# Optimization experiments

Measured on AMD Instinct MI355X. Metric: run time of the kernel, lower is better.

Reference implementation:

```python
import jax, jax.numpy as jnp
import numpy as np

L, H, NH, PF = 2, 256, 8, 512
D = H // NH
SCALE = float(np.sqrt(D))  # transformerCPI scales by sqrt(hid_dim // n_heads)


def layernorm(x, g, b, eps=1e-5):
    m = x.mean(-1, keepdims=True)
    v = ((x - m) ** 2).mean(-1, keepdims=True)
    return (x - m) / jnp.sqrt(v + eps) * g + b


def mha(q, k, v, wq, bq, wk, bk, wv, bv, wo, bo):
    B, Tq, _ = q.shape
    Tk = k.shape[1]
    Q = (q @ wq + bq).reshape(B, Tq, NH, D).transpose(0, 2, 1, 3)  # [B,h,Tq,d]
    K = (k @ wk + bk).reshape(B, Tk, NH, D).transpose(0, 2, 1, 3)
    V = (v @ wv + bv).reshape(B, Tk, NH, D).transpose(0, 2, 1, 3)
    att = jax.nn.softmax(jnp.einsum('bhqd,bhkd->bhqk', Q, K) / SCALE, axis=-1)
    x = jnp.einsum('bhqk,bhkd->bhqd', att, V).transpose(0, 2, 1, 3).reshape(B, Tq, H)
    return x @ wo + bo, att


def setup_inputs() -> dict:
    key = jax.random.key(0)
    ks = iter(jax.random.split(key, 64))
    B, T, S, A = 16, 512, 1024, 64
    p = lambda shape: jax.random.normal(next(ks), shape, jnp.float32) * 0.02
    inp = {
        'trg': jax.random.normal(next(ks), (B, T, A), jnp.float32),
        'src': jax.random.normal(next(ks), (B, S, H), jnp.float32),
        'ft_w': p((A, H)), 'ft_b': jnp.zeros((H,), jnp.float32),
        'fc1_w': p((H, 256)), 'fc1_b': jnp.zeros((256,), jnp.float32),
        'fc2_w': p((256, 2)), 'fc2_b': jnp.zeros((2,), jnp.float32),
        'ln_g': jnp.ones((L, H), jnp.float32), 'ln_b': jnp.zeros((L, H), jnp.float32),
        'pf_w1': p((L, H, PF)), 'pf_b1': jnp.zeros((L, PF), jnp.float32),
        'pf_w2': p((L, PF, H)), 'pf_b2': jnp.zeros((L, H), jnp.float32),
    }
    for pre in ('sa', 'ea'):
        for nm in ('q', 'k', 'v', 'o'):
            inp[f'{pre}_w{nm}'] = p((L, H, H))
            inp[f'{pre}_b{nm}'] = jnp.zeros((L, H), jnp.float32)
    return inp


def reference(trg, src, ft_w, ft_b, sa_wq, sa_bq, sa_wk, sa_bk, sa_wv, sa_bv, sa_wo, sa_bo,
              ea_wq, ea_bq, ea_wk, ea_bk, ea_wv, ea_bv, ea_wo, ea_bo,
              pf_w1, pf_b1, pf_w2, pf_b2, ln_g, ln_b, fc1_w, fc1_b, fc2_w, fc2_b):
    x = trg @ ft_w + ft_b  # [B,T,H]
    att = None
    for l in range(L):  # small fixed layer count
        sa_out, _ = mha(x, x, x, sa_wq[l], sa_bq[l], sa_wk[l], sa_bk[l],
                        sa_wv[l], sa_bv[l], sa_wo[l], sa_bo[l])
        x = layernorm(x + sa_out, ln_g[l], ln_b[l])
        ea_out, att = mha(x, src, src, ea_wq[l], ea_bq[l], ea_wk[l], ea_bk[l],
                          ea_wv[l], ea_bv[l], ea_wo[l], ea_bo[l])
        x = layernorm(x + ea_out, ln_g[l], ln_b[l])
        ff = jax.nn.relu(x @ pf_w1[l] + pf_b1[l]) @ pf_w2[l] + pf_b2[l]
        x = layernorm(x + ff, ln_g[l], ln_b[l])
    # norm-based softmax pooling (vectorized form of the original double loop)
    w = jax.nn.softmax(jnp.linalg.norm(x, axis=2), axis=1)  # [B,T]
    pooled = jnp.einsum('bt,bth->bh', w, x)                 # [B,H]
    label = jax.nn.relu(pooled @ fc1_w + fc1_b) @ fc2_w + fc2_b  # [B,2]
    return label, pooled, att
```

## Files before the change

kernel.cpp:

```cpp
#include <hip/hip_runtime.h>


typedef __bf16 bfrag __attribute__((ext_vector_type(8)));
typedef float f32x4 __attribute__((ext_vector_type(4)));
typedef unsigned int uint4v __attribute__((ext_vector_type(4)));

__device__ __forceinline__ unsigned short f2bf(float x) {
  unsigned u = __float_as_uint(x);
  u += 0x7fff + ((u >> 16) & 1);
  return (unsigned short)(u >> 16);
}
__device__ __forceinline__ float bf2f(unsigned short h) {
  return __uint_as_float((unsigned)h << 16);
}
__device__ __forceinline__ void split2(float x, unsigned short& hi, unsigned short& lo) {
  hi = f2bf(x);
  lo = f2bf(x - bf2f(hi));
}

__global__ __launch_bounds__(256) void wsplit(
    const float* __restrict__ W, short* __restrict__ Th, short* __restrict__ Tl,
    int K, int N)
{
  __shared__ float t[32][33];
  const int n0 = blockIdx.x * 32, k0 = blockIdx.y * 32;
  const int tx = threadIdx.x & 31, ty = threadIdx.x >> 5;
#pragma unroll
  for (int p = 0; p < 4; p++)
    t[ty + p * 8][tx] = W[(size_t)(k0 + ty + p * 8) * N + n0 + tx];
  __syncthreads();
#pragma unroll
  for (int p = 0; p < 4; p++) {
    float v = t[tx][ty + p * 8];
    unsigned short hi, lo; split2(v, hi, lo);
    size_t o = (size_t)(n0 + ty + p * 8) * K + k0 + tx;
    Th[o] = (short)hi; Tl[o] = (short)lo;
  }
}

__global__ __launch_bounds__(256) void xsplit(
    const float* __restrict__ X, short* __restrict__ Xh, short* __restrict__ Xl,
    int n4)
{
  int i = blockIdx.x * 256 + threadIdx.x;
  if (i < n4) {
    float4 v = ((const float4*)X)[i];
    ushort4 h, l;
    split2(v.x, h.x, l.x); split2(v.y, h.y, l.y);
    split2(v.z, h.z, l.z); split2(v.w, h.w, l.w);
    ((ushort4*)Xh)[i] = h; ((ushort4*)Xl)[i] = l;
  }
}

#define GEMM_CORE(Ah_g, Al_g, Bh_g, Bl_g, K)                                   \
  for (int k0 = 0; k0 < K; k0 += 32) {                                         \
    {                                                                          \
      const size_t ga = (size_t)(m0 + srow) * K + k0 + sc4 * 8;                \
      const size_t gb = (size_t)(n0 + srow) * K + k0 + sc4 * 8;                \
      uint4 va_h = *(const uint4*)(Ah_g + ga);                                 \
      uint4 va_l = *(const uint4*)(Al_g + ga);                                 \
      uint4 vb_h = *(const uint4*)(Bh_g + gb);                                 \
      uint4 vb_l = *(const uint4*)(Bl_g + gb);                                 \
      const int so = srow * 40 + sc4 * 8;                                      \
      *(uint4*)(Ah + so) = va_h;  *(uint4*)(Al + so) = va_l;                   \
      *(uint4*)(Bh + so) = vb_h;  *(uint4*)(Bl + so) = vb_l;                   \
    }                                                                          \
    __syncthreads();                                                           \
    bfrag af_h[2], af_l[2], bf_h[2], bf_l[2];                                  \
    _Pragma("unroll")                                                          \
    for (int mi = 0; mi < 2; mi++) {                                           \
      int r = wm * 32 + mi * 16 + l15;                                         \
      af_h[mi] = *(const bfrag*)(Ah + r * 40 + l4 * 8);                        \
      af_l[mi] = *(const bfrag*)(Al + r * 40 + l4 * 8);                        \
    }                                                                          \
    _Pragma("unroll")                                                          \
    for (int ni = 0; ni < 2; ni++) {                                           \
      int r = wn * 32 + ni * 16 + l15;                                         \
      bf_h[ni] = *(const bfrag*)(Bh + r * 40 + l4 * 8);                        \
      bf_l[ni] = *(const bfrag*)(Bl + r * 40 + l4 * 8);                        \
    }                                                                          \
    _Pragma("unroll")                                                          \
    for (int mi = 0; mi < 2; mi++)                                             \
      _Pragma("unroll")                                                        \
      for (int ni = 0; ni < 2; ni++) {                                         \
        acc[mi][ni] = __builtin_amdgcn_mfma_f32_16x16x32_bf16(af_h[mi], bf_h[ni], acc[mi][ni], 0, 0, 0); \
        acc[mi][ni] = __builtin_amdgcn_mfma_f32_16x16x32_bf16(af_h[mi], bf_l[ni], acc[mi][ni], 0, 0, 0); \
        acc[mi][ni] = __builtin_amdgcn_mfma_f32_16x16x32_bf16(af_l[mi], bf_h[ni], acc[mi][ni], 0, 0, 0); \
      }                                                                        \
    __syncthreads();                                                           \
  }

template <bool RELU, bool SPLIT, bool WRITE_C>
__global__ __launch_bounds__(256) void gemm_mfma(
    const short* __restrict__ Ah_g, const short* __restrict__ Al_g,
    const short* __restrict__ Bh_g, const short* __restrict__ Bl_g,
    const float* __restrict__ bias, float* __restrict__ C,
    short* __restrict__ Ch, short* __restrict__ Cl,
    int M, int N, int K)
{
  __shared__ short Ah[64 * 40], Al[64 * 40], Bh[64 * 40], Bl[64 * 40];
  const int tid = threadIdx.x;
  const int lane = tid & 63, w = tid >> 6;
  const int wm = w & 1, wn = w >> 1;
  const int m0 = blockIdx.x * 64, n0 = blockIdx.y * 64;
  const int srow = tid >> 2, sc4 = tid & 3;
  const int l15 = lane & 15, l4 = lane >> 4;
  f32x4 acc[2][2] = {};
  GEMM_CORE(Ah_g, Al_g, Bh_g, Bl_g, K)
#pragma unroll
  for (int mi = 0; mi < 2; mi++)
#pragma unroll
    for (int ni = 0; ni < 2; ni++) {
      const int n = n0 + wn * 32 + ni * 16 + l15;
      const float bv = bias[n];
#pragma unroll
      for (int r = 0; r < 4; r++) {
        const int m = m0 + wm * 32 + mi * 16 + l4 * 4 + r;
        float v = acc[mi][ni][r] + bv;
        if (RELU) v = fmaxf(v, 0.f);
        const size_t o = (size_t)m * N + n;
        if constexpr (WRITE_C) C[o] = v;
        if constexpr (SPLIT) {
          unsigned short hh, ll; split2(v, hh, ll);
          Ch[o] = (short)hh; Cl[o] = (short)ll;
        }
      }
    }
}

__global__ __launch_bounds__(256) void gemm_qkv(
    const short* __restrict__ Ah_g, const short* __restrict__ Al_g,
    const short* __restrict__ Bh_g, const short* __restrict__ Bl_g,
    const float* __restrict__ b0, const float* __restrict__ b1,
    const float* __restrict__ b2,
    short* __restrict__ D0h, short* __restrict__ D0l,
    short* __restrict__ D1h, short* __restrict__ D1l,
    short* __restrict__ D2h, short* __restrict__ D2l,
    int M, int K, int tksh, int nseg)
{
  __shared__ short Ah[64 * 40], Al[64 * 40], Bh[64 * 40], Bl[64 * 40];
  const int tid = threadIdx.x;
  const int lane = tid & 63, w = tid >> 6;
  const int wm = w & 1, wn = w >> 1;
  const int m0 = blockIdx.x * 64, n0 = blockIdx.y * 64;
  const int srow = tid >> 2, sc4 = tid & 3;
  const int l15 = lane & 15, l4 = lane >> 4;
  f32x4 acc[2][2] = {};
  GEMM_CORE(Ah_g, Al_g, Bh_g, Bl_g, K)
  const int seg = n0 >> 8;
  const bool vt = (seg == nseg - 1);
  const float* bias = (seg == 0) ? b0 : (seg == 1 ? b1 : b2);
  short* Ch = (seg == 0) ? D0h : (seg == 1 ? D1h : D2h);
  short* Cl = (seg == 0) ? D0l : (seg == 1 ? D1l : D2l);
#pragma unroll
  for (int mi = 0; mi < 2; mi++)
#pragma unroll
    for (int ni = 0; ni < 2; ni++) {
      const int n = n0 + wn * 32 + ni * 16 + l15;
      const int nl = n & 255;
      const float bv = bias[nl];
      if (vt) {
        const int m = m0 + wm * 32 + mi * 16 + l4 * 4;
        const int bb = m >> tksh, tt = m & ((1 << tksh) - 1);
        const size_t o = ((((size_t)bb * 8 + (nl >> 5)) * 32 + (nl & 31)) << tksh) + tt;
        unsigned long long wh = 0, wl = 0;
#pragma unroll
        for (int r = 0; r < 4; r++) {
          float v = acc[mi][ni][r] + bv;
          unsigned short hh, ll; split2(v, hh, ll);
          wh |= (unsigned long long)hh << (16 * r);
          wl |= (unsigned long long)ll << (16 * r);
        }
        *(unsigned long long*)(Ch + o) = wh;
        *(unsigned long long*)(Cl + o) = wl;
      } else {
#pragma unroll
        for (int r = 0; r < 4; r++) {
          const int m = m0 + wm * 32 + mi * 16 + l4 * 4 + r;
          float v = acc[mi][ni][r] + bv;
          unsigned short hh, ll; split2(v, hh, ll);
          const size_t o = (size_t)m * 256 + nl;
          Ch[o] = (short)hh; Cl[o] = (short)ll;
        }
      }
    }
}

template <int TK>
__global__ __launch_bounds__(512, 4) void attn_mfma(
    const short* __restrict__ Qh, const short* __restrict__ Ql,
    const short* __restrict__ Kh, const short* __restrict__ Kl,
    const short* __restrict__ Vth, const short* __restrict__ Vtl,
    short* __restrict__ Oh, short* __restrict__ Ol,
    float* __restrict__ att_out)
{
  __shared__ float sc[16 * TK];
  const int n = blockIdx.x;
  const int xcd = n & 7, ii = n >> 3;
  const int bh = xcd * 16 + (ii >> 5);
  const int q0 = (ii & 31) * 16;
  const int b = bh >> 3, h = bh & 7;
  const int tid = threadIdx.x;
  const int lane = tid & 63, w = tid >> 6;
  const int l15 = lane & 15, l4 = lane >> 4;
  const float inv_scale = 0.17677669529663687f;

  const size_t qbase = (((size_t)b * 512 + q0 + l15) * 8 + h) * 32 + l4 * 8;
  bfrag qh = *(const bfrag*)(Qh + qbase);
  bfrag ql = *(const bfrag*)(Ql + qbase);

#pragma unroll
  for (int t = 0; t < TK / 128; t++) {
    const int n0c = w * (TK / 8) + t * 16;
    const size_t kbase = (((size_t)b * TK + n0c + l15) * 8 + h) * 32 + l4 * 8;
    bfrag kh = *(const bfrag*)(Kh + kbase);
    bfrag kl = *(const bfrag*)(Kl + kbase);
    f32x4 acc = {};
    acc = __builtin_amdgcn_mfma_f32_16x16x32_bf16(qh, kh, acc, 0, 0, 0);
    acc = __builtin_amdgcn_mfma_f32_16x16x32_bf16(qh, kl, acc, 0, 0, 0);
    acc = __builtin_amdgcn_mfma_f32_16x16x32_bf16(ql, kh, acc, 0, 0, 0);
    const int col = n0c + l15;
#pragma unroll
    for (int r = 0; r < 4; r++) {
      const int row = l4 * 4 + r;
      sc[row * TK + ((((col >> 2) ^ (row & 7)) << 2) | (col & 3))] = acc[r] * inv_scale;
    }
  }
  __syncthreads();

  const int sr = tid >> 5, sj = tid & 31, srsw = sr & 7;
  float mx = -1e30f;
  for (int k = sj; k < TK; k += 32)
    mx = fmaxf(mx, sc[sr * TK + ((((k >> 2) ^ srsw) << 2) | (k & 3))]);
#pragma unroll
  for (int off = 16; off > 0; off >>= 1) mx = fmaxf(mx, __shfl_xor(mx, off, 32));
  float sum = 0.f;
  for (int k = sj; k < TK; k += 32) {
    const int idx = sr * TK + ((((k >> 2) ^ srsw) << 2) | (k & 3));
    float e = __expf(sc[idx] - mx);
    sc[idx] = e;
    sum += e;
  }
#pragma unroll
  for (int off = 16; off > 0; off >>= 1) sum += __shfl_xor(sum, off, 32);
  const float inv = 1.f / sum;
  __syncthreads();

  if (att_out) {
    const size_t orow = (((size_t)(b * 8 + h)) * 512 + q0 + sr) * TK;
#pragma unroll
    for (int t = 0; t < TK / 128; t++) {
      const int g = sj + 32 * t;
      float4 e4 = *(const float4*)&sc[sr * TK + ((g ^ srsw) << 2)];
      e4.x *= inv; e4.y *= inv; e4.z *= inv; e4.w *= inv;
      *(float4*)&att_out[orow + g * 4] = e4;
    }
  }

  f32x4 oa0 = {}, oa1 = {};
  const float* pr = sc + l15 * TK;
  const int psw = l15 & 7;
  const size_t vb0 = (((size_t)(b * 8 + h)) * 32 + l15) * TK;
#pragma unroll
  for (int kc = w * (TK / 8); kc < (w + 1) * (TK / 8); kc += 32) {
    const int g0 = (kc >> 2) + l4 * 2;
    float4 p0 = *(const float4*)(pr + ((g0 ^ psw) << 2));
    float4 p1 = *(const float4*)(pr + (((g0 + 1) ^ psw) << 2));
    float f[8] = {p0.x, p0.y, p0.z, p0.w, p1.x, p1.y, p1.z, p1.w};
    uint4v uh, ul;
#pragma unroll
    for (int i = 0; i < 4; i++) {
      unsigned short h0, l0, h1, l1;
      split2(f[2 * i], h0, l0); split2(f[2 * i + 1], h1, l1);
      uh[i] = (unsigned)h0 | ((unsigned)h1 << 16);
      ul[i] = (unsigned)l0 | ((unsigned)l1 << 16);
    }
    bfrag ph = __builtin_bit_cast(bfrag, uh);
    bfrag pl = __builtin_bit_cast(bfrag, ul);
    const size_t vk = vb0 + kc + l4 * 8;
    bfrag v0h = *(const bfrag*)(Vth + vk);
    bfrag v0l = *(const bfrag*)(Vtl + vk);
    bfrag v1h = *(const bfrag*)(Vth + vk + (size_t)16 * TK);
    bfrag v1l = *(const bfrag*)(Vtl + vk + (size_t)16 * TK);
    oa0 = __builtin_amdgcn_mfma_f32_16x16x32_bf16(ph, v0h, oa0, 0, 0, 0);
    oa0 = __builtin_amdgcn_mfma_f32_16x16x32_bf16(ph, v0l, oa0, 0, 0, 0);
    oa0 = __builtin_amdgcn_mfma_f32_16x16x32_bf16(pl, v0h, oa0, 0, 0, 0);
    oa1 = __builtin_amdgcn_mfma_f32_16x16x32_bf16(ph, v1h, oa1, 0, 0, 0);
    oa1 = __builtin_amdgcn_mfma_f32_16x16x32_bf16(ph, v1l, oa1, 0, 0, 0);
    oa1 = __builtin_amdgcn_mfma_f32_16x16x32_bf16(pl, v1h, oa1, 0, 0, 0);
  }
  __syncthreads();
  float* obuf = sc;
#pragma unroll
  for (int r = 0; r < 4; r++) {
    obuf[(w * 16 + l4 * 4 + r) * 33 + l15]      = oa0[r];
    obuf[(w * 16 + l4 * 4 + r) * 33 + 16 + l15] = oa1[r];
  }
  __syncthreads();
  {
    float s0 = 0.f;
#pragma unroll
    for (int ww = 0; ww < 8; ww++)
      s0 += obuf[(ww * 16 + sr) * 33 + sj];
    s0 *= inv;
    unsigned short h0, l0;
    split2(s0, h0, l0);
    const size_t ob = (((size_t)b * 512 + q0 + sr) * 8 + h) * 32 + sj;
    Oh[ob] = (short)h0;  Ol[ob] = (short)l0;
  }
}

__global__ __launch_bounds__(256) void residual_ln(
    float* __restrict__ x, const float* __restrict__ sub,
    const float* __restrict__ g, const float* __restrict__ bi,
    short* __restrict__ xh, short* __restrict__ xl)
{
  __shared__ float red[4];
  const size_t row = blockIdx.x;
  const int tid = threadIdx.x;
  float v = x[row * 256 + tid] + sub[row * 256 + tid];
  float s = v;
  for (int off = 32; off > 0; off >>= 1) s += __shfl_xor(s, off, 64);
  if ((tid & 63) == 0) red[tid >> 6] = s;
  __syncthreads();
  float mean = (red[0] + red[1] + red[2] + red[3]) * (1.f / 256.f);
  float d = v - mean;
  float s2 = d * d;
  for (int off = 32; off > 0; off >>= 1) s2 += __shfl_xor(s2, off, 64);
  __syncthreads();
  if ((tid & 63) == 0) red[tid >> 6] = s2;
  __syncthreads();
  float var = (red[0] + red[1] + red[2] + red[3]) * (1.f / 256.f);
  float y = d * rsqrtf(var + 1e-5f) * g[tid] + bi[tid];
  x[row * 256 + tid] = y;
  unsigned short hh, ll; split2(y, hh, ll);
  xh[row * 256 + tid] = (short)hh;
  xl[row * 256 + tid] = (short)ll;
}

__global__ __launch_bounds__(256) void row_norm(
    const float* __restrict__ x, float* __restrict__ nrm)
{
  __shared__ float red[4];
  const size_t row = blockIdx.x;
  const int tid = threadIdx.x;
  float v = x[row * 256 + tid];
  float s = v * v;
  for (int off = 32; off > 0; off >>= 1) s += __shfl_xor(s, off, 64);
  if ((tid & 63) == 0) red[tid >> 6] = s;
  __syncthreads();
  if (tid == 0) nrm[row] = sqrtf(red[0] + red[1] + red[2] + red[3]);
}

__global__ __launch_bounds__(256) void pool_kernel(
    const float* __restrict__ x, const float* __restrict__ nrm,
    float* __restrict__ pooled, float* __restrict__ pooled_out)
{
  __shared__ float w[512];
  __shared__ float red[4];
  const int b = blockIdx.x, tid = threadIdx.x;
  float n0 = nrm[b * 512 + tid], n1 = nrm[b * 512 + 256 + tid];
  float lm = fmaxf(n0, n1);
  for (int off = 32; off > 0; off >>= 1) lm = fmaxf(lm, __shfl_xor(lm, off, 64));
  if ((tid & 63) == 0) red[tid >> 6] = lm;
  __syncthreads();
  float m = fmaxf(fmaxf(red[0], red[1]), fmaxf(red[2], red[3]));
  float e0 = __expf(n0 - m), e1 = __expf(n1 - m);
  float ls = e0 + e1;
  for (int off = 32; off > 0; off >>= 1) ls += __shfl_xor(ls, off, 64);
  __syncthreads();
  if ((tid & 63) == 0) red[tid >> 6] = ls;
  __syncthreads();
  float inv = 1.f / (red[0] + red[1] + red[2] + red[3]);
  w[tid] = e0 * inv; w[tid + 256] = e1 * inv;
  __syncthreads();
  float acc = 0.f;
  for (int t = 0; t < 512; t++)
    acc += w[t] * x[((size_t)b * 512 + t) * 256 + tid];
  pooled[b * 256 + tid] = acc;
  pooled_out[b * 256 + tid] = acc;
}

__global__ __launch_bounds__(256) void fc_head(
    const float* __restrict__ pooled,
    const float* __restrict__ fc1_w, const float* __restrict__ fc1_b,
    const float* __restrict__ fc2_w, const float* __restrict__ fc2_b,
    float* __restrict__ label_out)
{
  __shared__ float pl[256];
  __shared__ float hid[256];
  const int b = blockIdx.x, tid = threadIdx.x;
  pl[tid] = pooled[b * 256 + tid];
  __syncthreads();
  float acc = fc1_b[tid];
  for (int k = 0; k < 256; k++)
    acc += pl[k] * fc1_w[k * 256 + tid];
  hid[tid] = fmaxf(acc, 0.f);
  __syncthreads();
  if (tid < 2) {
    float s = fc2_b[tid];
    for (int k = 0; k < 256; k++)
      s += hid[k] * fc2_w[k * 2 + tid];
    label_out[b * 2 + tid] = s;
  }
}

extern "C" void kernel_launch(void* const* d_in, const int* in_sizes, int n_in,
                              void* d_out, int out_size, void* d_ws, size_t ws_size,
                              hipStream_t stream)
{
  const float* trg   = (const float*)d_in[0];
  const float* src   = (const float*)d_in[1];
  const float* ft_w  = (const float*)d_in[2];
  const float* ft_b  = (const float*)d_in[3];
  const float* fc1_w = (const float*)d_in[4];
  const float* fc1_b = (const float*)d_in[5];
  const float* fc2_w = (const float*)d_in[6];
  const float* fc2_b = (const float*)d_in[7];
  const float* ln_g  = (const float*)d_in[8];
  const float* ln_b  = (const float*)d_in[9];
  const float* pf_w1 = (const float*)d_in[10];
  const float* pf_b1 = (const float*)d_in[11];
  const float* pf_w2 = (const float*)d_in[12];
  const float* pf_b2 = (const float*)d_in[13];
  const float* aw[2][8];
  for (int p = 0; p < 2; p++)
    for (int i = 0; i < 8; i++) aw[p][i] = (const float*)d_in[14 + p * 8 + i];
  float* outp = (float*)d_out;

  char* wsb = (char*)d_ws;
  const size_t MB = 1u << 20;
  float* x    = (float*)(wsb);
  float* sub  = (float*)(wsb + 8 * MB);
  short* x_hi = (short*)(wsb + 16 * MB);
  short* x_lo = (short*)(wsb + 20 * MB);
  short* qbh  = (short*)(wsb + 24 * MB);
  short* qbl  = (short*)(wsb + 28 * MB);
  short* kbh  = (short*)(wsb + 32 * MB);
  short* kbl  = (short*)(wsb + 40 * MB);
  short* vth  = (short*)(wsb + 48 * MB);
  short* vtl  = (short*)(wsb + 56 * MB);
  short* obh  = (short*)(wsb + 64 * MB);
  short* obl  = (short*)(wsb + 68 * MB);
  short* srch = (short*)(wsb + 72 * MB);
  short* srcl = (short*)(wsb + 80 * MB);
  short* w_hi = (short*)(wsb + 88 * MB);
  short* w_lo = (short*)(wsb + 92 * MB);
  short* ffmh = kbh;
  short* ffml = kbl;
  short* trgh = vth;
  short* trgl = vtl;
  float* nrm  = (float*)qbh;
  float* pld  = (float*)qbh + 8192;

  auto woff = [](int l, int idx) -> size_t {
    size_t base = 16384 + (size_t)l * 786432;
    if (idx < 8)  return base + (size_t)idx * 65536;
    if (idx == 8) return base + 524288;
    return base + 655360;
  };

  wsplit<<<dim3(8, 2), 256, 0, stream>>>(ft_w, w_hi, w_lo, 64, 256);
  for (int l = 0; l < 2; l++) {
    const size_t wo = (size_t)l * 65536;
    for (int i = 0; i < 4; i++)
      wsplit<<<dim3(8, 8), 256, 0, stream>>>(aw[0][2 * i] + wo,
          w_hi + woff(l, i), w_lo + woff(l, i), 256, 256);
    for (int i = 0; i < 4; i++)
      wsplit<<<dim3(8, 8), 256, 0, stream>>>(aw[1][2 * i] + wo,
          w_hi + woff(l, 4 + i), w_lo + woff(l, 4 + i), 256, 256);
    wsplit<<<dim3(16, 8), 256, 0, stream>>>(pf_w1 + (size_t)l * 131072,
        w_hi + woff(l, 8), w_lo + woff(l, 8), 256, 512);
    wsplit<<<dim3(8, 16), 256, 0, stream>>>(pf_w2 + (size_t)l * 131072,
        w_hi + woff(l, 9), w_lo + woff(l, 9), 512, 256);
  }
  xsplit<<<512, 256, 0, stream>>>(trg, trgh, trgl, 131072);
  xsplit<<<4096, 256, 0, stream>>>(src, srch, srcl, 1048576);

  gemm_mfma<false, true, true><<<dim3(128, 4), 256, 0, stream>>>(
      trgh, trgl, w_hi, w_lo, ft_b, x, x_hi, x_lo, 8192, 256, 64);

  for (int l = 0; l < 2; l++) {
    const size_t bo = (size_t)l * 256;
    gemm_qkv<<<dim3(128, 12), 256, 0, stream>>>(
        x_hi, x_lo, w_hi + woff(l, 0), w_lo + woff(l, 0),
        aw[0][1] + bo, aw[0][3] + bo, aw[0][5] + bo,
        qbh, qbl, kbh, kbl, vth, vtl, 8192, 256, 9, 3);
    attn_mfma<512><<<4096, 512, 0, stream>>>(
        qbh, qbl, kbh, kbl, vth, vtl, obh, obl, (float*)nullptr);
    gemm_mfma<false, false, true><<<dim3(128, 4), 256, 0, stream>>>(
        obh, obl, w_hi + woff(l, 3), w_lo + woff(l, 3), aw[0][7] + bo,
        sub, nullptr, nullptr, 8192, 256, 256);
    residual_ln<<<8192, 256, 0, stream>>>(x, sub, ln_g + bo, ln_b + bo, x_hi, x_lo);
    gemm_mfma<false, true, false><<<dim3(128, 4), 256, 0, stream>>>(
        x_hi, x_lo, w_hi + woff(l, 4), w_lo + woff(l, 4), aw[1][1] + bo,
        nullptr, qbh, qbl, 8192, 256, 256);
    gemm_qkv<<<dim3(256, 8), 256, 0, stream>>>(
        srch, srcl, w_hi + woff(l, 5), w_lo + woff(l, 5),
        aw[1][3] + bo, aw[1][5] + bo, nullptr,
        kbh, kbl, vth, vtl, nullptr, nullptr, 16384, 256, 10, 2);
    {
      float* att = (l == 1) ? (outp + 4128) : (float*)nullptr;
      attn_mfma<1024><<<4096, 512, 0, stream>>>(
          qbh, qbl, kbh, kbl, vth, vtl, obh, obl, att);
    }
    gemm_mfma<false, false, true><<<dim3(128, 4), 256, 0, stream>>>(
        obh, obl, w_hi + woff(l, 7), w_lo + woff(l, 7), aw[1][7] + bo,
        sub, nullptr, nullptr, 8192, 256, 256);
    residual_ln<<<8192, 256, 0, stream>>>(x, sub, ln_g + bo, ln_b + bo, x_hi, x_lo);
    gemm_mfma<true, true, false><<<dim3(128, 8), 256, 0, stream>>>(
        x_hi, x_lo, w_hi + woff(l, 8), w_lo + woff(l, 8), pf_b1 + (size_t)l * 512,
        nullptr, ffmh, ffml, 8192, 512, 256);
    gemm_mfma<false, false, true><<<dim3(128, 4), 256, 0, stream>>>(
        ffmh, ffml, w_hi + woff(l, 9), w_lo + woff(l, 9), pf_b2 + bo,
        sub, nullptr, nullptr, 8192, 256, 512);
    residual_ln<<<8192, 256, 0, stream>>>(x, sub, ln_g + bo, ln_b + bo, x_hi, x_lo);
  }

  row_norm<<<8192, 256, 0, stream>>>(x, nrm);
  pool_kernel<<<16, 256, 0, stream>>>(x, nrm, pld, outp + 32);
  fc_head<<<16, 256, 0, stream>>>(pld, fc1_w, fc1_b, fc2_w, fc2_b, outp);
}
```

Before: 1.085 ms.

## Enlarge GEMM tiles to 128x128 with direct LDS loads, batch weight splits, fuse norm

GEMM kernels move from 64x64 to 128x128 tiles, with each wave computing a 64x64 sub-tile, and stage global data straight into LDS through global_load_lds. The goal is more operand reuse and fewer register round trips. All weight-split launches are merged into one descriptor-driven kernel, and residual layernorm now uses one wave per row with float4 accesses and no LDS reductions. The final layernorm also computes the row norm, which removes the row_norm kernel, and pooling is split across chunks to use more blocks. The larger tiles cut the GEMM grid to 128-256 blocks, so occupancy and CU coverage may suffer. The unpadded LDS layout may also cause bank conflicts.

```diff
diff --git a/kernel.cpp b/kernel.cpp
--- a/kernel.cpp
+++ b/kernel.cpp
@@ -18,12 +18,29 @@
   lo = f2bf(x - bf2f(hi));
 }
 
-__global__ __launch_bounds__(256) void wsplit(
-    const float* __restrict__ W, short* __restrict__ Th, short* __restrict__ Tl,
-    int K, int N)
+__device__ __forceinline__ void load16_lds(const short* g, short* l) {
+  __builtin_amdgcn_global_load_lds(
+      (const __attribute__((address_space(1))) unsigned int*)g,
+      (__attribute__((address_space(3))) unsigned int*)l, 16, 0, 0);
+}
+
+struct WDesc { const float* src; long long dst; int K; int N; int tile0; int pad; };
+struct WAll { WDesc d[21]; };
+
+__global__ __launch_bounds__(256) void wsplit_all(
+    WAll P, short* __restrict__ Th, short* __restrict__ Tl)
 {
   __shared__ float t[32][33];
-  const int n0 = blockIdx.x * 32, k0 = blockIdx.y * 32;
+  const int bid = blockIdx.x;
+  int i = 0;
+  while (i < 20 && bid >= P.d[i + 1].tile0) i++;
+  const float* __restrict__ W = P.d[i].src;
+  const int K = P.d[i].K, N = P.d[i].N;
+  const int lt = bid - P.d[i].tile0;
+  const int ntn = N >> 5;
+  const int n0 = (lt % ntn) * 32, k0 = (lt / ntn) * 32;
+  short* th = Th + P.d[i].dst;
+  short* tl = Tl + P.d[i].dst;
   const int tx = threadIdx.x & 31, ty = threadIdx.x >> 5;
 #pragma unroll
   for (int p = 0; p < 4; p++)
@@ -34,7 +51,7 @@
     float v = t[tx][ty + p * 8];
     unsigned short hi, lo; split2(v, hi, lo);
     size_t o = (size_t)(n0 + ty + p * 8) * K + k0 + tx;
-    Th[o] = (short)hi; Tl[o] = (short)lo;
+    th[o] = (short)hi; tl[o] = (short)lo;
   }
 }
 
@@ -52,40 +69,40 @@
   }
 }
 
-#define GEMM_CORE(Ah_g, Al_g, Bh_g, Bl_g, K)                                   \
+#define GEMM128_CORE(Ah_g, Al_g, Bh_g, Bl_g, K)                                \
   for (int k0 = 0; k0 < K; k0 += 32) {                                         \
-    {                                                                          \
-      const size_t ga = (size_t)(m0 + srow) * K + k0 + sc4 * 8;                \
-      const size_t gb = (size_t)(n0 + srow) * K + k0 + sc4 * 8;                \
-      uint4 va_h = *(const uint4*)(Ah_g + ga);                                 \
-      uint4 va_l = *(const uint4*)(Al_g + ga);                                 \
-      uint4 vb_h = *(const uint4*)(Bh_g + gb);                                 \
-      uint4 vb_l = *(const uint4*)(Bl_g + gb);                                 \
-      const int so = srow * 40 + sc4 * 8;                                      \
-      *(uint4*)(Ah + so) = va_h;  *(uint4*)(Al + so) = va_l;                   \
-      *(uint4*)(Bh + so) = vb_h;  *(uint4*)(Bl + so) = vb_l;                   \
+    _Pragma("unroll")                                                          \
+    for (int i = 0; i < 2; i++) {                                              \
+      const int row = i * 64 + w * 16 + srow;                                  \
+      const size_t ga = (size_t)(m0 + row) * K + k0 + sc4 * 8;                 \
+      const size_t gb = (size_t)(n0 + row) * K + k0 + sc4 * 8;                 \
+      const int ldst = i * 2048 + w * 512;                                     \
+      load16_lds(Ah_g + ga, &Asl[0][ldst]);                                    \
+      load16_lds(Al_g + ga, &Asl[1][ldst]);                                    \
+      load16_lds(Bh_g + gb, &Bsl[0][ldst]);                                    \
+      load16_lds(Bl_g + gb, &Bsl[1][ldst]);                                    \
     }                                                                          \
     __syncthreads();                                                           \
-    bfrag af_h[2], af_l[2], bf_h[2], bf_l[2];                                  \
+    bfrag afh[4], afl[4], bfh[4], bfl[4];                                      \
     _Pragma("unroll")                                                          \
-    for (int mi = 0; mi < 2; mi++) {                                           \
-      int r = wm * 32 + mi * 16 + l15;                                         \
-      af_h[mi] = *(const bfrag*)(Ah + r * 40 + l4 * 8);                        \
-      af_l[mi] = *(const bfrag*)(Al + r * 40 + l4 * 8);                        \
+    for (int mi = 0; mi < 4; mi++) {                                           \
+      const int r = wm * 64 + mi * 16 + l15;                                   \
+      afh[mi] = *(const bfrag*)(&Asl[0][r * 32 + l4 * 8]);                     \
+      afl[mi] = *(const bfrag*)(&Asl[1][r * 32 + l4 * 8]);                     \
     }                                                                          \
     _Pragma("unroll")                                                          \
-    for (int ni = 0; ni < 2; ni++) {                                           \
-      int r = wn * 32 + ni * 16 + l15;                                         \
-      bf_h[ni] = *(const bfrag*)(Bh + r * 40 + l4 * 8);                        \
-      bf_l[ni] = *(const bfrag*)(Bl + r * 40 + l4 * 8);                        \
+    for (int ni = 0; ni < 4; ni++) {                                           \
+      const int r = wn * 64 + ni * 16 + l15;                                   \
+      bfh[ni] = *(const bfrag*)(&Bsl[0][r * 32 + l4 * 8]);                     \
+      bfl[ni] = *(const bfrag*)(&Bsl[1][r * 32 + l4 * 8]);                     \
     }                                                                          \
     _Pragma("unroll")                                                          \
-    for (int mi = 0; mi < 2; mi++)                                             \
+    for (int mi = 0; mi < 4; mi++)                                             \
       _Pragma("unroll")                                                        \
-      for (int ni = 0; ni < 2; ni++) {                                         \
-        acc[mi][ni] = __builtin_amdgcn_mfma_f32_16x16x32_bf16(af_h[mi], bf_h[ni], acc[mi][ni], 0, 0, 0); \
-        acc[mi][ni] = __builtin_amdgcn_mfma_f32_16x16x32_bf16(af_h[mi], bf_l[ni], acc[mi][ni], 0, 0, 0); \
-        acc[mi][ni] = __builtin_amdgcn_mfma_f32_16x16x32_bf16(af_l[mi], bf_h[ni], acc[mi][ni], 0, 0, 0); \
+      for (int ni = 0; ni < 4; ni++) {                                         \
+        acc[mi][ni] = __builtin_amdgcn_mfma_f32_16x16x32_bf16(afh[mi], bfh[ni], acc[mi][ni], 0, 0, 0); \
+        acc[mi][ni] = __builtin_amdgcn_mfma_f32_16x16x32_bf16(afh[mi], bfl[ni], acc[mi][ni], 0, 0, 0); \
+        acc[mi][ni] = __builtin_amdgcn_mfma_f32_16x16x32_bf16(afl[mi], bfh[ni], acc[mi][ni], 0, 0, 0); \
       }                                                                        \
     __syncthreads();                                                           \
   }
@@ -98,24 +115,25 @@
     short* __restrict__ Ch, short* __restrict__ Cl,
     int M, int N, int K)
 {
-  __shared__ short Ah[64 * 40], Al[64 * 40], Bh[64 * 40], Bl[64 * 40];
+  __shared__ short Asl[2][128 * 32];
+  __shared__ short Bsl[2][128 * 32];
   const int tid = threadIdx.x;
   const int lane = tid & 63, w = tid >> 6;
   const int wm = w & 1, wn = w >> 1;
-  const int m0 = blockIdx.x * 64, n0 = blockIdx.y * 64;
-  const int srow = tid >> 2, sc4 = tid & 3;
+  const int m0 = blockIdx.x * 128, n0 = blockIdx.y * 128;
+  const int srow = lane >> 2, sc4 = lane & 3;
   const int l15 = lane & 15, l4 = lane >> 4;
-  f32x4 acc[2][2] = {};
-  GEMM_CORE(Ah_g, Al_g, Bh_g, Bl_g, K)
-#pragma unroll
-  for (int mi = 0; mi < 2; mi++)
-#pragma unroll
-    for (int ni = 0; ni < 2; ni++) {
-      const int n = n0 + wn * 32 + ni * 16 + l15;
+  f32x4 acc[4][4] = {};
+  GEMM128_CORE(Ah_g, Al_g, Bh_g, Bl_g, K)
+#pragma unroll
+  for (int mi = 0; mi < 4; mi++)
+#pragma unroll
+    for (int ni = 0; ni < 4; ni++) {
+      const int n = n0 + wn * 64 + ni * 16 + l15;
       const float bv = bias[n];
 #pragma unroll
       for (int r = 0; r < 4; r++) {
-        const int m = m0 + wm * 32 + mi * 16 + l4 * 4 + r;
+        const int m = m0 + wm * 64 + mi * 16 + l4 * 4 + r;
         float v = acc[mi][ni][r] + bv;
         if (RELU) v = fmaxf(v, 0.f);
         const size_t o = (size_t)m * N + n;
@@ -138,29 +156,30 @@
     short* __restrict__ D2h, short* __restrict__ D2l,
     int M, int K, int tksh, int nseg)
 {
-  __shared__ short Ah[64 * 40], Al[64 * 40], Bh[64 * 40], Bl[64 * 40];
+  __shared__ short Asl[2][128 * 32];
+  __shared__ short Bsl[2][128 * 32];
   const int tid = threadIdx.x;
   const int lane = tid & 63, w = tid >> 6;
   const int wm = w & 1, wn = w >> 1;
-  const int m0 = blockIdx.x * 64, n0 = blockIdx.y * 64;
-  const int srow = tid >> 2, sc4 = tid & 3;
+  const int m0 = blockIdx.x * 128, n0 = blockIdx.y * 128;
+  const int srow = lane >> 2, sc4 = lane & 3;
   const int l15 = lane & 15, l4 = lane >> 4;
-  f32x4 acc[2][2] = {};
-  GEMM_CORE(Ah_g, Al_g, Bh_g, Bl_g, K)
+  f32x4 acc[4][4] = {};
+  GEMM128_CORE(Ah_g, Al_g, Bh_g, Bl_g, K)
   const int seg = n0 >> 8;
   const bool vt = (seg == nseg - 1);
   const float* bias = (seg == 0) ? b0 : (seg == 1 ? b1 : b2);
   short* Ch = (seg == 0) ? D0h : (seg == 1 ? D1h : D2h);
   short* Cl = (seg == 0) ? D0l : (seg == 1 ? D1l : D2l);
 #pragma unroll
-  for (int mi = 0; mi < 2; mi++)
-#pragma unroll
-    for (int ni = 0; ni < 2; ni++) {
-      const int n = n0 + wn * 32 + ni * 16 + l15;
+  for (int mi = 0; mi < 4; mi++)
+#pragma unroll
+    for (int ni = 0; ni < 4; ni++) {
+      const int n = n0 + wn * 64 + ni * 16 + l15;
       const int nl = n & 255;
       const float bv = bias[nl];
       if (vt) {
-        const int m = m0 + wm * 32 + mi * 16 + l4 * 4;
+        const int m = m0 + wm * 64 + mi * 16 + l4 * 4;
         const int bb = m >> tksh, tt = m & ((1 << tksh) - 1);
         const size_t o = ((((size_t)bb * 8 + (nl >> 5)) * 32 + (nl & 31)) << tksh) + tt;
         unsigned long long wh = 0, wl = 0;
@@ -176,7 +195,7 @@
       } else {
 #pragma unroll
         for (int r = 0; r < 4; r++) {
-          const int m = m0 + wm * 32 + mi * 16 + l4 * 4 + r;
+          const int m = m0 + wm * 64 + mi * 16 + l4 * 4 + r;
           float v = acc[mi][ni][r] + bv;
           unsigned short hh, ll; split2(v, hh, ll);
           const size_t o = (size_t)m * 256 + nl;
@@ -310,55 +329,53 @@
   }
 }
 
+template <bool WNORM>
 __global__ __launch_bounds__(256) void residual_ln(
     float* __restrict__ x, const float* __restrict__ sub,
     const float* __restrict__ g, const float* __restrict__ bi,
-    short* __restrict__ xh, short* __restrict__ xl)
-{
-  __shared__ float red[4];
-  const size_t row = blockIdx.x;
-  const int tid = threadIdx.x;
-  float v = x[row * 256 + tid] + sub[row * 256 + tid];
-  float s = v;
+    short* __restrict__ xh, short* __restrict__ xl, float* __restrict__ nrm)
+{
+  const int wid = threadIdx.x >> 6, lane = threadIdx.x & 63;
+  const size_t row = (size_t)blockIdx.x * 4 + wid;
+  const int c = lane * 4;
+  float4 xv = *(const float4*)&x[row * 256 + c];
+  float4 sv = *(const float4*)&sub[row * 256 + c];
+  float v0 = xv.x + sv.x, v1 = xv.y + sv.y, v2 = xv.z + sv.z, v3 = xv.w + sv.w;
+  float s = v0 + v1 + v2 + v3;
+#pragma unroll
   for (int off = 32; off > 0; off >>= 1) s += __shfl_xor(s, off, 64);
-  if ((tid & 63) == 0) red[tid >> 6] = s;
-  __syncthreads();
-  float mean = (red[0] + red[1] + red[2] + red[3]) * (1.f / 256.f);
-  float d = v - mean;
-  float s2 = d * d;
+  const float mean = s * (1.f / 256.f);
+  const float d0 = v0 - mean, d1 = v1 - mean, d2 = v2 - mean, d3 = v3 - mean;
+  float s2 = d0 * d0 + d1 * d1 + d2 * d2 + d3 * d3;
+#pragma unroll
   for (int off = 32; off > 0; off >>= 1) s2 += __shfl_xor(s2, off, 64);
-  __syncthreads();
-  if ((tid & 63) == 0) red[tid >> 6] = s2;
-  __syncthreads();
-  float var = (red[0] + red[1] + red[2] + red[3]) * (1.f / 256.f);
-  float y = d * rsqrtf(var + 1e-5f) * g[tid] + bi[tid];
-  x[row * 256 + tid] = y;
-  unsigned short hh, ll; split2(y, hh, ll);
-  xh[row * 256 + tid] = (short)hh;
-  xl[row * 256 + tid] = (short)ll;
-}
-
-__global__ __launch_bounds__(256) void row_norm(
-    const float* __restrict__ x, float* __restrict__ nrm)
-{
-  __shared__ float red[4];
-  const size_t row = blockIdx.x;
-  const int tid = threadIdx.x;
-  float v = x[row * 256 + tid];
-  float s = v * v;
-  for (int off = 32; off > 0; off >>= 1) s += __shfl_xor(s, off, 64);
-  if ((tid & 63) == 0) red[tid >> 6] = s;
-  __syncthreads();
-  if (tid == 0) nrm[row] = sqrtf(red[0] + red[1] + red[2] + red[3]);
-}
-
-__global__ __launch_bounds__(256) void pool_kernel(
+  const float rs = rsqrtf(s2 * (1.f / 256.f) + 1e-5f);
+  const float4 gv = *(const float4*)&g[c];
+  const float4 bv = *(const float4*)&bi[c];
+  const float y0 = d0 * rs * gv.x + bv.x, y1 = d1 * rs * gv.y + bv.y;
+  const float y2 = d2 * rs * gv.z + bv.z, y3 = d3 * rs * gv.w + bv.w;
+  float4 yo; yo.x = y0; yo.y = y1; yo.z = y2; yo.w = y3;
+  *(float4*)&x[row * 256 + c] = yo;
+  ushort4 hh, ll;
+  split2(y0, hh.x, ll.x); split2(y1, hh.y, ll.y);
+  split2(y2, hh.z, ll.z); split2(y3, hh.w, ll.w);
+  *(ushort4*)&xh[row * 256 + c] = hh;
+  *(ushort4*)&xl[row * 256 + c] = ll;
+  if (WNORM) {
+    float ns = y0 * y0 + y1 * y1 + y2 * y2 + y3 * y3;
+#pragma unroll
+    for (int off = 32; off > 0; off >>= 1) ns += __shfl_xor(ns, off, 64);
+    if (lane == 0) nrm[row] = sqrtf(ns);
+  }
+}
+
+__global__ __launch_bounds__(256) void pool1(
     const float* __restrict__ x, const float* __restrict__ nrm,
-    float* __restrict__ pooled, float* __restrict__ pooled_out)
+    float* __restrict__ partial)
 {
   __shared__ float w[512];
   __shared__ float red[4];
-  const int b = blockIdx.x, tid = threadIdx.x;
+  const int b = blockIdx.x, cchunk = blockIdx.y, tid = threadIdx.x;
   float n0 = nrm[b * 512 + tid], n1 = nrm[b * 512 + 256 + tid];
   float lm = fmaxf(n0, n1);
   for (int off = 32; off > 0; off >>= 1) lm = fmaxf(lm, __shfl_xor(lm, off, 64));
@@ -375,10 +392,23 @@
   w[tid] = e0 * inv; w[tid + 256] = e1 * inv;
   __syncthreads();
   float acc = 0.f;
-  for (int t = 0; t < 512; t++)
+  const int t0 = cchunk * 128;
+  for (int t = t0; t < t0 + 128; t++)
     acc += w[t] * x[((size_t)b * 512 + t) * 256 + tid];
-  pooled[b * 256 + tid] = acc;
-  pooled_out[b * 256 + tid] = acc;
+  partial[((size_t)b * 4 + cchunk) * 256 + tid] = acc;
+}
+
+__global__ __launch_bounds__(256) void pool2(
+    const float* __restrict__ partial, float* __restrict__ pooled,
+    float* __restrict__ pooled_out)
+{
+  const int b = blockIdx.x, tid = threadIdx.x;
+  float s = partial[((size_t)b * 4 + 0) * 256 + tid]
+          + partial[((size_t)b * 4 + 1) * 256 + tid]
+          + partial[((size_t)b * 4 + 2) * 256 + tid]
+          + partial[((size_t)b * 4 + 3) * 256 + tid];
+  pooled[b * 256 + tid] = s;
+  pooled_out[b * 256 + tid] = s;
 }
 
 __global__ __launch_bounds__(256) void fc_head(
@@ -452,6 +482,7 @@
   short* trgl = vtl;
   float* nrm  = (float*)qbh;
   float* pld  = (float*)qbh + 8192;
+  float* part = (float*)qbh + 16384;
 
   auto woff = [](int l, int idx) -> size_t {
     size_t base = 16384 + (size_t)l * 786432;
@@ -460,42 +491,47 @@
     return base + 655360;
   };
 
-  wsplit<<<dim3(8, 2), 256, 0, stream>>>(ft_w, w_hi, w_lo, 64, 256);
-  for (int l = 0; l < 2; l++) {
-    const size_t wo = (size_t)l * 65536;
-    for (int i = 0; i < 4; i++)
-      wsplit<<<dim3(8, 8), 256, 0, stream>>>(aw[0][2 * i] + wo,
-          w_hi + woff(l, i), w_lo + woff(l, i), 256, 256);
-    for (int i = 0; i < 4; i++)
-      wsplit<<<dim3(8, 8), 256, 0, stream>>>(aw[1][2 * i] + wo,
-          w_hi + woff(l, 4 + i), w_lo + woff(l, 4 + i), 256, 256);
-    wsplit<<<dim3(16, 8), 256, 0, stream>>>(pf_w1 + (size_t)l * 131072,
-        w_hi + woff(l, 8), w_lo + woff(l, 8), 256, 512);
-    wsplit<<<dim3(8, 16), 256, 0, stream>>>(pf_w2 + (size_t)l * 131072,
-        w_hi + woff(l, 9), w_lo + woff(l, 9), 512, 256);
+  {
+    WAll P{};
+    int t = 0, e = 0;
+    auto add = [&](const float* s, int K, int N, size_t dst) {
+      P.d[e].src = s; P.d[e].dst = (long long)dst;
+      P.d[e].K = K; P.d[e].N = N; P.d[e].tile0 = t;
+      t += (K / 32) * (N / 32); e++;
+    };
+    add(ft_w, 64, 256, 0);
+    for (int l = 0; l < 2; l++) {
+      const size_t wo = (size_t)l * 65536;
+      for (int i = 0; i < 4; i++) add(aw[0][2 * i] + wo, 256, 256, woff(l, i));
+      for (int i = 0; i < 4; i++) add(aw[1][2 * i] + wo, 256, 256, woff(l, 4 + i));
+      add(pf_w1 + (size_t)l * 131072, 256, 512, woff(l, 8));
+      add(pf_w2 + (size_t)l * 131072, 512, 256, woff(l, 9));
+    }
+    wsplit_all<<<t, 256, 0, stream>>>(P, w_hi, w_lo);
   }
   xsplit<<<512, 256, 0, stream>>>(trg, trgh, trgl, 131072);
   xsplit<<<4096, 256, 0, stream>>>(src, srch, srcl, 1048576);
 
-  gemm_mfma<false, true, true><<<dim3(128, 4), 256, 0, stream>>>(
+  gemm_mfma<false, true, true><<<dim3(64, 2), 256, 0, stream>>>(
       trgh, trgl, w_hi, w_lo, ft_b, x, x_hi, x_lo, 8192, 256, 64);
 
   for (int l = 0; l < 2; l++) {
     const size_t bo = (size_t)l * 256;
-    gemm_qkv<<<dim3(128, 12), 256, 0, stream>>>(
+    gemm_qkv<<<dim3(64, 6), 256, 0, stream>>>(
         x_hi, x_lo, w_hi + woff(l, 0), w_lo + woff(l, 0),
         aw[0][1] + bo, aw[0][3] + bo, aw[0][5] + bo,
         qbh, qbl, kbh, kbl, vth, vtl, 8192, 256, 9, 3);
     attn_mfma<512><<<4096, 512, 0, stream>>>(
         qbh, qbl, kbh, kbl, vth, vtl, obh, obl, (float*)nullptr);
-    gemm_mfma<false, false, true><<<dim3(128, 4), 256, 0, stream>>>(
+    gemm_mfma<false, false, true><<<dim3(64, 2), 256, 0, stream>>>(
         obh, obl, w_hi + woff(l, 3), w_lo + woff(l, 3), aw[0][7] + bo,
         sub, nullptr, nullptr, 8192, 256, 256);
-    residual_ln<<<8192, 256, 0, stream>>>(x, sub, ln_g + bo, ln_b + bo, x_hi, x_lo);
-    gemm_mfma<false, true, false><<<dim3(128, 4), 256, 0, stream>>>(
+    residual_ln<false><<<2048, 256, 0, stream>>>(x, sub, ln_g + bo, ln_b + bo,
+                                                 x_hi, x_lo, nullptr);
+    gemm_mfma<false, true, false><<<dim3(64, 2), 256, 0, stream>>>(
         x_hi, x_lo, w_hi + woff(l, 4), w_lo + woff(l, 4), aw[1][1] + bo,
         nullptr, qbh, qbl, 8192, 256, 256);
-    gemm_qkv<<<dim3(256, 8), 256, 0, stream>>>(
+    gemm_qkv<<<dim3(128, 4), 256, 0, stream>>>(
         srch, srcl, w_hi + woff(l, 5), w_lo + woff(l, 5),
         aw[1][3] + bo, aw[1][5] + bo, nullptr,
         kbh, kbl, vth, vtl, nullptr, nullptr, 16384, 256, 10, 2);
@@ -504,20 +540,27 @@
       attn_mfma<1024><<<4096, 512, 0, stream>>>(
           qbh, qbl, kbh, kbl, vth, vtl, obh, obl, att);
     }
-    gemm_mfma<false, false, true><<<dim3(128, 4), 256, 0, stream>>>(
+    gemm_mfma<false, false, true><<<dim3(64, 2), 256, 0, stream>>>(
         obh, obl, w_hi + woff(l, 7), w_lo + woff(l, 7), aw[1][7] + bo,
         sub, nullptr, nullptr, 8192, 256, 256);
-    residual_ln<<<8192, 256, 0, stream>>>(x, sub, ln_g + bo, ln_b + bo, x_hi, x_lo);
-    gemm_mfma<true, true, false><<<dim3(128, 8), 256, 0, stream>>>(
+    residual_ln<false><<<2048, 256, 0, stream>>>(x, sub, ln_g + bo, ln_b + bo,
+                                                 x_hi, x_lo, nullptr);
+    gemm_mfma<true, true, false><<<dim3(64, 4), 256, 0, stream>>>(
         x_hi, x_lo, w_hi + woff(l, 8), w_lo + woff(l, 8), pf_b1 + (size_t)l * 512,
         nullptr, ffmh, ffml, 8192, 512, 256);
-    gemm_mfma<false, false, true><<<dim3(128, 4), 256, 0, stream>>>(
+    gemm_mfma<false, false, true><<<dim3(64, 2), 256, 0, stream>>>(
         ffmh, ffml, w_hi + woff(l, 9), w_lo + woff(l, 9), pf_b2 + bo,
         sub, nullptr, nullptr, 8192, 256, 512);
-    residual_ln<<<8192, 256, 0, stream>>>(x, sub, ln_g + bo, ln_b + bo, x_hi, x_lo);
-  }
-
-  row_norm<<<8192, 256, 0, stream>>>(x, nrm);
-  pool_kernel<<<16, 256, 0, stream>>>(x, nrm, pld, outp + 32);
+    if (l == 0) {
+      residual_ln<false><<<2048, 256, 0, stream>>>(x, sub, ln_g + bo, ln_b + bo,
+                                                   x_hi, x_lo, nullptr);
+    } else {
+      residual_ln<true><<<2048, 256, 0, stream>>>(x, sub, ln_g + bo, ln_b + bo,
+                                                  x_hi, x_lo, nrm);
+    }
+  }
+
+  pool1<<<dim3(16, 4), 256, 0, stream>>>(x, nrm, part);
+  pool2<<<16, 256, 0, stream>>>(part, pld, outp + 32);
   fc_head<<<16, 256, 0, stream>>>(pld, fc1_w, fc1_b, fc2_w, fc2_b, outp);
 }
```

Result: no change. 1.068 ms (-1.6%).
